# Performance work log

Measured on AMD Instinct MI355X. Metric: run time of the kernel, lower is better.

The kernel has to match this reference:

```python
import jax, jax.numpy as jnp
import numpy as np

N_NODES = 100000
N_EDGES = 1600000
N_GRAPHS = 1024
N_FEAT = 128
HID = 64
N_CLASSES = 16
N_CENT = 3  # centroids per class


def setup_inputs() -> dict:
    key = jax.random.key(0)
    ks = jax.random.split(key, 8)
    x = jax.random.normal(ks[0], (N_NODES, N_FEAT), dtype=jnp.float32)
    edge_index = jax.random.randint(ks[1], (2, N_EDGES), 0, N_NODES, dtype=jnp.int64)
    batch = jnp.sort(jax.random.randint(ks[2], (N_NODES,), 0, N_GRAPHS, dtype=jnp.int64))
    s = 1.0 / np.sqrt(N_FEAT)
    W1 = jax.random.normal(ks[3], (N_FEAT, HID), dtype=jnp.float32) * s
    W2 = jax.random.normal(ks[4], (HID, HID), dtype=jnp.float32) * (1.0 / np.sqrt(HID))
    W3 = jax.random.normal(ks[5], (HID, HID), dtype=jnp.float32) * (1.0 / np.sqrt(HID))
    b1 = jnp.zeros((HID,), jnp.float32)
    b2 = jnp.zeros((HID,), jnp.float32)
    b3 = jnp.zeros((HID,), jnp.float32)
    centroids = jax.random.normal(ks[6], (N_CLASSES * N_CENT, HID), dtype=jnp.float32)
    reject_bias = jnp.zeros((1,), jnp.float32)
    return {"x": x, "edge_index": edge_index, "batch": batch,
            "W1": W1, "b1": b1, "W2": W2, "b2": b2, "W3": W3, "b3": b3,
            "centroids": centroids, "reject_bias": reject_bias}


def _gcn_conv(x, W, b, src, dst, norm, n_nodes):
    # PyG GCNConv: out[dst] = sum_e norm_e * (x[src_e] @ W), + bias
    h = x @ W                      # [N, out]
    msg = h[src] * norm[:, None]   # [E+N, out] gather + scale
    out = jax.ops.segment_sum(msg, dst, num_segments=n_nodes)
    return out + b


def reference(x, edge_index, batch, W1, b1, W2, b2, W3, b3, centroids, reject_bias):
    n = x.shape[0]
    loops = jnp.arange(n, dtype=edge_index.dtype)
    src = jnp.concatenate([edge_index[0], loops])
    dst = jnp.concatenate([edge_index[1], loops])
    # symmetric normalization on A + I
    deg = jax.ops.segment_sum(jnp.ones_like(dst, dtype=x.dtype), dst, num_segments=n)
    dinv = jax.lax.rsqrt(jnp.maximum(deg, 1.0))
    norm = dinv[src] * dinv[dst]

    h = jax.nn.relu(_gcn_conv(x, W1, b1, src, dst, norm, n))  # dropout is identity at eval
    h = jax.nn.relu(_gcn_conv(h, W2, b2, src, dst, norm, n))
    h = _gcn_conv(h, W3, b3, src, dst, norm, n)

    # global mean pool over graphs in the batch
    summ = jax.ops.segment_sum(h, batch, num_segments=N_GRAPHS)          # [G, HID]
    cnt = jax.ops.segment_sum(jnp.ones((n,), h.dtype), batch, num_segments=N_GRAPHS)
    emb = summ / jnp.maximum(cnt, 1.0)[:, None]

    # centroid distance head: squared euclidean to all class centroids
    d = (jnp.sum(emb * emb, -1, keepdims=True)
         - 2.0 * emb @ centroids.T
         + jnp.sum(centroids * centroids, -1))                           # [G, 16*3]
    d_pc = jnp.min(d.reshape(-1, N_CLASSES, N_CENT), axis=-1)            # [G, 16]
    class_logits = -d_pc
    reject_logit = jnp.min(d_pc, axis=-1, keepdims=True) - reject_bias   # [G, 1]
    return jnp.concatenate([class_logits, reject_logit], axis=-1)        # [G, 17]
```

## Files before the change

### kernel.cpp

```cpp
#include <hip/hip_runtime.h>

#define HID 64
#define NCLS 16
#define NCENT 3
#define NCENTS (NCLS * NCENT)
#define BSHIFT 9
#define BINW (1 << BSHIFT)
#define NBINMAX 256
#define CHUNK 4096
#define EPT (CHUNK / 256)
#define NU 8

static inline int ceil_div(int a, int b) { return (a + b - 1) / b; }

__device__ inline unsigned short f2bf(float f) {
    unsigned int u = __float_as_uint(f);
    return (unsigned short)((u + 0x7FFFu + ((u >> 16) & 1u)) >> 16);
}
__device__ inline unsigned int pack2bf(float lo, float hi) {
    return (unsigned int)f2bf(lo) | ((unsigned int)f2bf(hi) << 16);
}
__device__ inline float bf2f(unsigned short h) {
    return __uint_as_float(((unsigned int)h) << 16);
}
__device__ inline float bflo(unsigned int u) { return __uint_as_float(u << 16); }
__device__ inline float bfhi(unsigned int u) { return __uint_as_float(u & 0xFFFF0000u); }

typedef short bf16x8 __attribute__((ext_vector_type(8)));
typedef float f32x4 __attribute__((ext_vector_type(4)));


__device__ void wprep_one(const float* __restrict__ W, unsigned short* __restrict__ Wh,
                          unsigned short* __restrict__ Wl, int K) {
    for (int idx = threadIdx.x; idx < K * 64; idx += 256) {
        int k = idx >> 6, colc = idx & 63;
        float f = W[idx];
        unsigned short h = f2bf(f);
        unsigned short lo = f2bf(f - bf2f(h));
        int kt = k >> 5, kin = k & 31, ct = colc >> 4;
        int ln = ((kin >> 3) << 4) | (colc & 15);
        int o = (((kt * 4 + ct) * 64) + ln) * 8 + (kin & 7);
        Wh[o] = h; Wl[o] = lo;
    }
}


__global__ void k_count_w(const int* __restrict__ dst, int* __restrict__ binCnt,
                          int E, int nbins,
                          const float* __restrict__ W1, const float* __restrict__ W2,
                          const float* __restrict__ W3,
                          unsigned short* __restrict__ W1h, unsigned short* __restrict__ W1l,
                          unsigned short* __restrict__ W2h, unsigned short* __restrict__ W2l,
                          unsigned short* __restrict__ W3h, unsigned short* __restrict__ W3l) {
    if (blockIdx.x >= gridDim.x - 3) {
        int w = blockIdx.x - (gridDim.x - 3);
        if (w == 0) wprep_one(W1, W1h, W1l, 128);
        else if (w == 1) wprep_one(W2, W2h, W2l, 64);
        else wprep_one(W3, W3h, W3l, 64);
        return;
    }
    __shared__ int c[NBINMAX];
    for (int i = threadIdx.x; i < nbins; i += 256) c[i] = 0;
    __syncthreads();
    int e = blockIdx.x * CHUNK + threadIdx.x;
#pragma unroll
    for (int j = 0; j < EPT; j++, e += 256)
        if (e < E) atomicAdd(&c[dst[e] >> BSHIFT], 1);
    __syncthreads();
    for (int i = threadIdx.x; i < nbins; i += 256)
        if (c[i] > 0) atomicAdd(&binCnt[i], c[i]);
}

__global__ void k_binoff(const int* __restrict__ binCnt, int* __restrict__ binBase,
                         int nbins, int E) {
    __shared__ int ts[NBINMAX];
    int t = threadIdx.x;
    int v = (t < nbins) ? binCnt[t] : 0;
    ts[t] = v;
    __syncthreads();
    for (int off = 1; off < NBINMAX; off <<= 1) {
        int x = (t >= off) ? ts[t - off] : 0;
        __syncthreads();
        ts[t] += x;
        __syncthreads();
    }
    if (t < nbins) binBase[t] = ts[t] - v;
    if (t == 0) binBase[nbins] = E;
}

__global__ __launch_bounds__(256) void k_bin(const int* __restrict__ src,
                                             const int* __restrict__ dst,
                                             const int* __restrict__ binBase,
                                             int* __restrict__ binCur,
                                             int2* __restrict__ binned,
                                             int E, int nbins) {
    __shared__ int cnt[NBINMAX], off[NBINMAX], gbase[NBINMAX];
    __shared__ int2 stage[CHUNK];
    const int c0 = blockIdx.x * CHUNK;
    const int tid = threadIdx.x;
    cnt[tid] = 0;
    __syncthreads();
    int sv[EPT], dv[EPT];
#pragma unroll
    for (int j = 0; j < EPT; j++) {
        int e = c0 + j * 256 + tid;
        dv[j] = -1;
        if (e < E) {
            sv[j] = src[e];
            dv[j] = dst[e];
            atomicAdd(&cnt[dv[j] >> BSHIFT], 1);
        }
    }
    __syncthreads();
    off[tid] = cnt[tid];
    __syncthreads();
    for (int o = 1; o < NBINMAX; o <<= 1) {
        int x = (tid >= o) ? off[tid - o] : 0;
        __syncthreads();
        off[tid] += x;
        __syncthreads();
    }
    int excl = off[tid] - cnt[tid];
    __syncthreads();
    off[tid] = excl;
    gbase[tid] = (tid < nbins && cnt[tid] > 0) ? atomicAdd(&binCur[tid], cnt[tid]) : 0;
    cnt[tid] = 0;
    __syncthreads();
#pragma unroll
    for (int j = 0; j < EPT; j++)
        if (dv[j] >= 0) {
            int b = dv[j] >> BSHIFT;
            int pos = off[b] + atomicAdd(&cnt[b], 1);
            stage[pos] = make_int2(sv[j], dv[j]);
        }
    __syncthreads();
    int tot = min(CHUNK, E - c0);
    for (int i = tid; i < tot; i += 256) {
        int2 v = stage[i];
        int b = v.y >> BSHIFT;
        binned[binBase[b] + gbase[b] + (i - off[b])] = v;
    }
}

__global__ __launch_bounds__(256) void k_fillc2(const int2* __restrict__ binned,
                                                const int* __restrict__ binBase,
                                                int* __restrict__ col,
                                                int* __restrict__ rs_out,
                                                int* __restrict__ deg_out,
                                                float* __restrict__ dinv_out, int N) {
    __shared__ int c[BINW];
    __shared__ int rsl[BINW];
    __shared__ int ts[256];
    int b = blockIdx.x;
    int s = binBase[b], e = binBase[b + 1];
    int n0 = b << BSHIFT;
    int t = threadIdx.x;
    c[2 * t] = 0; c[2 * t + 1] = 0;
    __syncthreads();
    for (int i = s + t; i < e; i += 256)
        atomicAdd(&c[binned[i].y - n0], 1);
    __syncthreads();
    int v0 = c[2 * t], v1 = c[2 * t + 1];
    ts[t] = v0 + v1;
    __syncthreads();
    for (int off = 1; off < 256; off <<= 1) {
        int x = (t >= off) ? ts[t - off] : 0;
        __syncthreads();
        ts[t] += x;
        __syncthreads();
    }
    int base = binBase[b] + ts[t] - (v0 + v1);
    rsl[2 * t] = base;
    rsl[2 * t + 1] = base + v0;
    int n = n0 + 2 * t;
    if (n < N) {
        deg_out[n] = v0; rs_out[n] = base;
        dinv_out[n] = rsqrtf((float)(v0 + 1));
    }
    if (n + 1 < N) {
        deg_out[n + 1] = v1; rs_out[n + 1] = base + v0;
        dinv_out[n + 1] = rsqrtf((float)(v1 + 1));
    }
    c[2 * t] = 0; c[2 * t + 1] = 0;
    __syncthreads();
    for (int i = s + t; i < e; i += 256) {
        int2 v = binned[i];
        int lo = v.y - n0;
        int pos = rsl[lo] + atomicAdd(&c[lo], 1);
        col[pos] = v.x;
    }
}


template <int K>
__global__ __launch_bounds__(256) void k_gemm_mfma(const float* __restrict__ Ain,
                                                   const unsigned short* __restrict__ Wh,
                                                   const unsigned short* __restrict__ Wl,
                                                   unsigned short* __restrict__ out,
                                                   const float* __restrict__ dinv, int N) {
    const int lane = threadIdx.x & 63;
    const int wave = threadIdx.x >> 6;
    const int row0 = blockIdx.x * 64 + wave * 16;
    int arow = row0 + (lane & 15);
    if (arow > N - 1) arow = N - 1;
    const int kb = (lane >> 4) * 8;

    f32x4 acc[4] = {};

#pragma unroll
    for (int kt = 0; kt < K / 32; ++kt) {
        bf16x8 ah, al;
        const float* ap = Ain + (size_t)arow * K + kt * 32 + kb;
        float4 f0 = *(const float4*)ap;
        float4 f1 = *(const float4*)(ap + 4);
        float fv[8] = {f0.x, f0.y, f0.z, f0.w, f1.x, f1.y, f1.z, f1.w};
#pragma unroll
        for (int j = 0; j < 8; ++j) {
            unsigned short h = f2bf(fv[j]);
            ah[j] = (short)h;
            al[j] = (short)f2bf(fv[j] - bf2f(h));
        }
#pragma unroll
        for (int ct = 0; ct < 4; ++ct) {
            const size_t wo = ((size_t)(kt * 4 + ct) * 64 + lane) * 8;
            bf16x8 wh = *(const bf16x8*)(Wh + wo);
            bf16x8 wl = *(const bf16x8*)(Wl + wo);
            acc[ct] = __builtin_amdgcn_mfma_f32_16x16x32_bf16(ah, wh, acc[ct], 0, 0, 0);
            acc[ct] = __builtin_amdgcn_mfma_f32_16x16x32_bf16(al, wh, acc[ct], 0, 0, 0);
            acc[ct] = __builtin_amdgcn_mfma_f32_16x16x32_bf16(ah, wl, acc[ct], 0, 0, 0);
        }
    }

    const int rb = row0 + (lane >> 4) * 4;
    const int cb = lane & 15;
#pragma unroll
    for (int i = 0; i < 4; ++i) {
        int row = rb + i;
        if (row < N) {
            float d = dinv[row];
#pragma unroll
            for (int ct = 0; ct < 4; ++ct)
                out[(size_t)row * HID + ct * 16 + cb] = f2bf(d * acc[ct][i]);
        }
    }
}


__global__ __launch_bounds__(256) void k_aggf(const unsigned short* __restrict__ tin,
                                              unsigned short* __restrict__ tout,
                                              const int* __restrict__ rs,
                                              const int* __restrict__ deg,
                                              const int* __restrict__ col,
                                              const float* __restrict__ dinv,
                                              const float* __restrict__ bias,
                                              const unsigned short* __restrict__ Wh,
                                              const unsigned short* __restrict__ Wl,
                                              int N) {
    __shared__ unsigned int tl[32][36];
    const int tid = threadIdx.x;
    const int lane = tid & 63;
    const int wave = tid >> 6;
    const int group = tid >> 3;
    const int l = tid & 7;
    int node = blockIdx.x * 32 + group;
    int cnode = node < N ? node : N - 1;

    float di = dinv[cnode];
    uint4 tb = ((const uint4*)(tin + (size_t)cnode * HID))[l];
    float a0 = bflo(tb.x), a1 = bfhi(tb.x);
    float a2 = bflo(tb.y), a3 = bfhi(tb.y);
    float a4 = bflo(tb.z), a5 = bfhi(tb.z);
    float a6 = bflo(tb.w), a7 = bfhi(tb.w);

    int beg = rs[cnode];
    int cnt = deg[cnode];
    int last = beg + cnt - 1;
    const int gbase = lane & 56;
    for (int e = 0; e < cnt; e += NU) {
        int idx = beg + e + l;
        int cv = col[idx < last ? idx : last];
        int sv[NU];
#pragma unroll
        for (int j = 0; j < NU; j++) sv[j] = __shfl(cv, gbase + j, 64);
        uint4 vv[NU];
#pragma unroll
        for (int j = 0; j < NU; j++) vv[j] = ((const uint4*)(tin + (size_t)sv[j] * HID))[l];
#pragma unroll
        for (int j = 0; j < NU; j++) {
            a0 += bflo(vv[j].x); a1 += bfhi(vv[j].x);
            a2 += bflo(vv[j].y); a3 += bfhi(vv[j].y);
            a4 += bflo(vv[j].z); a5 += bfhi(vv[j].z);
            a6 += bflo(vv[j].w); a7 += bfhi(vv[j].w);
        }
    }
    int pad = (NU - (cnt & (NU - 1))) & (NU - 1);
    if (cnt > 0 && pad > 0) {
        float fp = (float)pad;
        uint4 vl = ((const uint4*)(tin + (size_t)col[last] * HID))[l];
        a0 = fmaf(-fp, bflo(vl.x), a0); a1 = fmaf(-fp, bfhi(vl.x), a1);
        a2 = fmaf(-fp, bflo(vl.y), a2); a3 = fmaf(-fp, bfhi(vl.y), a3);
        a4 = fmaf(-fp, bflo(vl.z), a4); a5 = fmaf(-fp, bfhi(vl.z), a5);
        a6 = fmaf(-fp, bflo(vl.w), a6); a7 = fmaf(-fp, bfhi(vl.w), a7);
    }
    float4 b0 = ((const float4*)bias)[2 * l];
    float4 b1 = ((const float4*)bias)[2 * l + 1];
    a0 = fmaxf(fmaf(di, a0, b0.x), 0.f); a1 = fmaxf(fmaf(di, a1, b0.y), 0.f);
    a2 = fmaxf(fmaf(di, a2, b0.z), 0.f); a3 = fmaxf(fmaf(di, a3, b0.w), 0.f);
    a4 = fmaxf(fmaf(di, a4, b1.x), 0.f); a5 = fmaxf(fmaf(di, a5, b1.y), 0.f);
    a6 = fmaxf(fmaf(di, a6, b1.z), 0.f); a7 = fmaxf(fmaf(di, a7, b1.w), 0.f);

    uint4 o;
    o.x = pack2bf(a0, a1); o.y = pack2bf(a2, a3);
    o.z = pack2bf(a4, a5); o.w = pack2bf(a6, a7);
    *(uint4*)&tl[group][4 * l] = o;
    __syncthreads();

    const int row0 = (wave >> 1) * 16;
    const int ctb = (wave & 1) * 2;
    const int arow = row0 + (lane & 15);
    const int am = lane >> 4;

    f32x4 acc[2] = {};
#pragma unroll
    for (int kt = 0; kt < 2; ++kt) {
        bf16x8 ah = *(const bf16x8*)&tl[arow][kt * 16 + 4 * am];
#pragma unroll
        for (int c = 0; c < 2; ++c) {
            const size_t wo = ((size_t)(kt * 4 + ctb + c) * 64 + lane) * 8;
            bf16x8 wh = *(const bf16x8*)(Wh + wo);
            bf16x8 wl = *(const bf16x8*)(Wl + wo);
            acc[c] = __builtin_amdgcn_mfma_f32_16x16x32_bf16(ah, wh, acc[c], 0, 0, 0);
            acc[c] = __builtin_amdgcn_mfma_f32_16x16x32_bf16(ah, wl, acc[c], 0, 0, 0);
        }
    }

    const int rb = row0 + (lane >> 4) * 4;
    const int cb = lane & 15;
#pragma unroll
    for (int i = 0; i < 4; ++i) {
        int gnode = blockIdx.x * 32 + rb + i;
        if (gnode < N) {
            float d2 = dinv[gnode];
#pragma unroll
            for (int c = 0; c < 2; ++c)
                tout[(size_t)gnode * HID + (ctb + c) * 16 + cb] = f2bf(d2 * acc[c][i]);
        }
    }
}


__global__ void k_agg(const unsigned short* __restrict__ tin,
                      unsigned short* __restrict__ out,
                      const int* __restrict__ rs, const int* __restrict__ deg,
                      const int* __restrict__ col,
                      const float* __restrict__ dinv, const float* __restrict__ bias,
                      int N) {
    int node = (blockIdx.x * blockDim.x + threadIdx.x) >> 3;
    int l = threadIdx.x & 7;
    if (node >= N) return;
    int lane = threadIdx.x & 63;
    float di = dinv[node];
    uint4 tb = ((const uint4*)(tin + (size_t)node * HID))[l];
    float a0 = bflo(tb.x), a1 = bfhi(tb.x);
    float a2 = bflo(tb.y), a3 = bfhi(tb.y);
    float a4 = bflo(tb.z), a5 = bfhi(tb.z);
    float a6 = bflo(tb.w), a7 = bfhi(tb.w);

    int beg = rs[node];
    int cnt = deg[node];
    int last = beg + cnt - 1;
    const int gbase = lane & 56;
    for (int e = 0; e < cnt; e += NU) {
        int idx = beg + e + l;
        int cv = col[idx < last ? idx : last];
        int sv[NU];
#pragma unroll
        for (int j = 0; j < NU; j++) sv[j] = __shfl(cv, gbase + j, 64);
        uint4 vv[NU];
#pragma unroll
        for (int j = 0; j < NU; j++) vv[j] = ((const uint4*)(tin + (size_t)sv[j] * HID))[l];
#pragma unroll
        for (int j = 0; j < NU; j++) {
            a0 += bflo(vv[j].x); a1 += bfhi(vv[j].x);
            a2 += bflo(vv[j].y); a3 += bfhi(vv[j].y);
            a4 += bflo(vv[j].z); a5 += bfhi(vv[j].z);
            a6 += bflo(vv[j].w); a7 += bfhi(vv[j].w);
        }
    }
    int pad = (NU - (cnt & (NU - 1))) & (NU - 1);
    if (cnt > 0 && pad > 0) {
        float fp = (float)pad;
        uint4 vl = ((const uint4*)(tin + (size_t)col[last] * HID))[l];
        a0 = fmaf(-fp, bflo(vl.x), a0); a1 = fmaf(-fp, bfhi(vl.x), a1);
        a2 = fmaf(-fp, bflo(vl.y), a2); a3 = fmaf(-fp, bfhi(vl.y), a3);
        a4 = fmaf(-fp, bflo(vl.z), a4); a5 = fmaf(-fp, bfhi(vl.z), a5);
        a6 = fmaf(-fp, bflo(vl.w), a6); a7 = fmaf(-fp, bfhi(vl.w), a7);
    }
    float4 b0 = ((const float4*)bias)[2 * l];
    float4 b1 = ((const float4*)bias)[2 * l + 1];
    a0 = fmaf(di, a0, b0.x); a1 = fmaf(di, a1, b0.y);
    a2 = fmaf(di, a2, b0.z); a3 = fmaf(di, a3, b0.w);
    a4 = fmaf(di, a4, b1.x); a5 = fmaf(di, a5, b1.y);
    a6 = fmaf(di, a6, b1.z); a7 = fmaf(di, a7, b1.w);
    uint4 o;
    o.x = pack2bf(a0, a1); o.y = pack2bf(a2, a3);
    o.z = pack2bf(a4, a5); o.w = pack2bf(a6, a7);
    ((uint4*)(out + (size_t)node * HID))[l] = o;
}


__global__ void k_pool_head(const unsigned short* __restrict__ h,
                            const int* __restrict__ batch,
                            const float* __restrict__ cent, const float* __restrict__ rbias,
                            float* __restrict__ out, int N) {
    int g = blockIdx.x;
    int lo = 0, hi = N;
    while (lo < hi) { int mid = (lo + hi) >> 1; if (batch[mid] < g) lo = mid + 1; else hi = mid; }
    int s = lo;
    lo = 0; hi = N;
    while (lo < hi) { int mid = (lo + hi) >> 1; if (batch[mid] < g + 1) lo = mid + 1; else hi = mid; }
    int e = lo;

    __shared__ float part[4][HID];
    __shared__ float embS[HID];
    __shared__ float dS[NCENTS];
    __shared__ float dpcS[NCLS];

    int lane = threadIdx.x & 63, wid = threadIdx.x >> 6;
    float acc = 0.0f;
    for (int i = s + wid; i < e; i += 4) acc += bf2f(h[(size_t)i * HID + lane]);
    part[wid][lane] = acc;
    __syncthreads();
    if (wid == 0) {
        float v = part[0][lane] + part[1][lane] + part[2][lane] + part[3][lane];
        embS[lane] = v / fmaxf((float)(e - s), 1.0f);
    }
    __syncthreads();
    if (threadIdx.x < NCENTS) {
        const float* c = cent + threadIdx.x * HID;
        float d = 0.0f;
        for (int k = 0; k < HID; k++) { float df = embS[k] - c[k]; d = fmaf(df, df, d); }
        dS[threadIdx.x] = d;
    }
    __syncthreads();
    if (threadIdx.x < NCLS) {
        float m = fminf(dS[threadIdx.x * 3],
                        fminf(dS[threadIdx.x * 3 + 1], dS[threadIdx.x * 3 + 2]));
        dpcS[threadIdx.x] = m;
        out[g * (NCLS + 1) + threadIdx.x] = -m;
    }
    __syncthreads();
    if (threadIdx.x == 0) {
        float m = dpcS[0];
        for (int i = 1; i < NCLS; i++) m = fminf(m, dpcS[i]);
        out[g * (NCLS + 1) + NCLS] = m - rbias[0];
    }
}


extern "C" void kernel_launch(void* const* d_in, const int* in_sizes, int n_in,
                              void* d_out, int out_size, void* d_ws, size_t ws_size,
                              hipStream_t stream) {
    const float* x    = (const float*)d_in[0];
    const int*   ei   = (const int*)d_in[1];
    const int*   bat  = (const int*)d_in[2];
    const float* W1   = (const float*)d_in[3];
    const float* b1   = (const float*)d_in[4];
    const float* W2   = (const float*)d_in[5];
    const float* b2   = (const float*)d_in[6];
    const float* W3   = (const float*)d_in[7];
    const float* b3   = (const float*)d_in[8];
    const float* cent = (const float*)d_in[9];
    const float* rb   = (const float*)d_in[10];
    float* out = (float*)d_out;

    const int N = in_sizes[0] / 128;
    const int E = in_sizes[1] / 2;
    const int nbins = (N + BINW - 1) >> BSHIFT;

    char* p = (char*)d_ws;
    unsigned short* T0 = (unsigned short*)p; p += (size_t)N * HID * 2;
    unsigned short* T1 = (unsigned short*)p; p += (size_t)N * HID * 2;
    int2*  binned = (int2*)p;  p += (size_t)E * 8;
    int*   col    = (int*)p;   p += (size_t)E * 4;
    float* dinv   = (float*)p; p += (size_t)N * 4;
    int*   rs     = (int*)p;   p += (size_t)N * 4;
    int*   deg    = (int*)p;   p += (size_t)N * 4;
    int*   binBase= (int*)p;   p += (NBINMAX + 2) * 4;
    int*   binCnt = (int*)p;   p += NBINMAX * 4;
    int*   binCur = (int*)p;   p += NBINMAX * 4;
    p = (char*)(((uintptr_t)p + 15) & ~(uintptr_t)15);
    unsigned short* W1h = (unsigned short*)p; p += 8192 * 2;
    unsigned short* W1l = (unsigned short*)p; p += 8192 * 2;
    unsigned short* W2h = (unsigned short*)p; p += 4096 * 2;
    unsigned short* W2l = (unsigned short*)p; p += 4096 * 2;
    unsigned short* W3h = (unsigned short*)p; p += 4096 * 2;
    unsigned short* W3l = (unsigned short*)p; p += 4096 * 2;

    hipMemsetAsync(binCnt, 0, 2 * NBINMAX * 4, stream);

    const int nEB = ceil_div(E, CHUNK);
    k_count_w<<<nEB + 3, 256, 0, stream>>>(ei + E, binCnt, E, nbins,
                                           W1, W2, W3, W1h, W1l, W2h, W2l, W3h, W3l);
    k_binoff<<<1, 256, 0, stream>>>(binCnt, binBase, nbins, E);
    k_bin<<<nEB, 256, 0, stream>>>(ei, ei + E, binBase, binCur, binned, E, nbins);
    k_fillc2<<<nbins, 256, 0, stream>>>(binned, binBase, col, rs, deg, dinv, N);

    k_gemm_mfma<128><<<ceil_div(N, 64), 256, 0, stream>>>(x, W1h, W1l, T0, dinv, N);
    k_aggf<<<ceil_div(N, 32), 256, 0, stream>>>(T0, T1, rs, deg, col, dinv, b1, W2h, W2l, N);
    k_aggf<<<ceil_div(N, 32), 256, 0, stream>>>(T1, T0, rs, deg, col, dinv, b2, W3h, W3l, N);
    k_agg<<<ceil_div(N * 8, 256), 256, 0, stream>>>(T0, T1, rs, deg, col, dinv, b3, N);

    k_pool_head<<<1024, 256, 0, stream>>>(T1, bat, cent, rb, out, N);
}
```

Baseline: 307.4 us.

## Sort nodes by degree for load-balanced aggregation and prefetch next column indices

Builds a degree histogram during CSR fill, scans it, and scatters nodes into a degree-sorted permutation. The aggregation kernels then process nodes in that order, so the 8 node groups in a wavefront have similar edge counts and less loop divergence. The aggregation loop also prefetches the next chunk of column indices before the feature gathers. In exchange it adds two small kernels plus an extra indirection, and destroys the spatial locality of writes and self-feature reads.

```diff
diff --git a/kernel.cpp b/kernel.cpp
--- a/kernel.cpp
+++ b/kernel.cpp
@@ -10,6 +10,7 @@
 #define CHUNK 4096
 #define EPT (CHUNK / 256)
 #define NU 8
+#define NDB 64
 
 static inline int ceil_div(int a, int b) { return (a + b - 1) / b; }
 
@@ -147,15 +148,18 @@
                                                 int* __restrict__ col,
                                                 int* __restrict__ rs_out,
                                                 int* __restrict__ deg_out,
-                                                float* __restrict__ dinv_out, int N) {
+                                                float* __restrict__ dinv_out,
+                                                int* __restrict__ degHist, int N) {
     __shared__ int c[BINW];
     __shared__ int rsl[BINW];
     __shared__ int ts[256];
+    __shared__ int dh[NDB];
     int b = blockIdx.x;
     int s = binBase[b], e = binBase[b + 1];
     int n0 = b << BSHIFT;
     int t = threadIdx.x;
     c[2 * t] = 0; c[2 * t + 1] = 0;
+    if (t < NDB) dh[t] = 0;
     __syncthreads();
     for (int i = s + t; i < e; i += 256)
         atomicAdd(&c[binned[i].y - n0], 1);
@@ -176,10 +180,12 @@
     if (n < N) {
         deg_out[n] = v0; rs_out[n] = base;
         dinv_out[n] = rsqrtf((float)(v0 + 1));
+        atomicAdd(&dh[v0 < NDB - 1 ? v0 : NDB - 1], 1);
     }
     if (n + 1 < N) {
         deg_out[n + 1] = v1; rs_out[n + 1] = base + v0;
         dinv_out[n + 1] = rsqrtf((float)(v1 + 1));
+        atomicAdd(&dh[v1 < NDB - 1 ? v1 : NDB - 1], 1);
     }
     c[2 * t] = 0; c[2 * t + 1] = 0;
     __syncthreads();
@@ -188,6 +194,50 @@
         int lo = v.y - n0;
         int pos = rsl[lo] + atomicAdd(&c[lo], 1);
         col[pos] = v.x;
+    }
+    __syncthreads();
+    if (t < NDB && dh[t] > 0) atomicAdd(&degHist[t], dh[t]);
+}
+
+
+__global__ void k_dscan(const int* __restrict__ degHist, int* __restrict__ bucketCur) {
+    __shared__ int ts[NDB];
+    int t = threadIdx.x;
+    int v = degHist[t];
+    ts[t] = v;
+    __syncthreads();
+    for (int o = 1; o < NDB; o <<= 1) {
+        int x = (t >= o) ? ts[t - o] : 0;
+        __syncthreads();
+        ts[t] += x;
+        __syncthreads();
+    }
+    bucketCur[t] = ts[t] - v;
+}
+
+
+__global__ __launch_bounds__(256) void k_pscatter(const int* __restrict__ deg,
+                                                  int* __restrict__ bucketCur,
+                                                  int* __restrict__ perm, int N) {
+    __shared__ int cnt[NDB], gb[NDB];
+    int t = threadIdx.x;
+    int node = blockIdx.x * 256 + t;
+    if (t < NDB) cnt[t] = 0;
+    __syncthreads();
+    int d = -1;
+    if (node < N) {
+        d = deg[node]; d = d < NDB - 1 ? d : NDB - 1;
+        atomicAdd(&cnt[d], 1);
+    }
+    __syncthreads();
+    if (t < NDB) {
+        gb[t] = cnt[t] > 0 ? atomicAdd(&bucketCur[t], cnt[t]) : 0;
+        cnt[t] = 0;
+    }
+    __syncthreads();
+    if (node < N) {
+        int pos = gb[d] + atomicAdd(&cnt[d], 1);
+        perm[pos] = node;
     }
 }
 
@@ -255,6 +305,7 @@
                                               const float* __restrict__ bias,
                                               const unsigned short* __restrict__ Wh,
                                               const unsigned short* __restrict__ Wl,
+                                              const int* __restrict__ perm,
                                               int N) {
     __shared__ unsigned int tl[32][36];
     const int tid = threadIdx.x;
@@ -262,8 +313,8 @@
     const int wave = tid >> 6;
     const int group = tid >> 3;
     const int l = tid & 7;
-    int node = blockIdx.x * 32 + group;
-    int cnode = node < N ? node : N - 1;
+    int gi = blockIdx.x * 32 + group;
+    int cnode = perm[gi < N ? gi : N - 1];
 
     float di = dinv[cnode];
     uint4 tb = ((const uint4*)(tin + (size_t)cnode * HID))[l];
@@ -276,15 +327,18 @@
     int cnt = deg[cnode];
     int last = beg + cnt - 1;
     const int gbase = lane & 56;
+    int pidx = beg + l;
+    int cv = (cnt > 0) ? col[pidx < last ? pidx : last] : 0;
     for (int e = 0; e < cnt; e += NU) {
-        int idx = beg + e + l;
-        int cv = col[idx < last ? idx : last];
         int sv[NU];
 #pragma unroll
         for (int j = 0; j < NU; j++) sv[j] = __shfl(cv, gbase + j, 64);
+        int nidx = beg + e + NU + l;
+        int cvn = col[nidx < last ? nidx : last];
         uint4 vv[NU];
 #pragma unroll
         for (int j = 0; j < NU; j++) vv[j] = ((const uint4*)(tin + (size_t)sv[j] * HID))[l];
+        cv = cvn;
 #pragma unroll
         for (int j = 0; j < NU; j++) {
             a0 += bflo(vv[j].x); a1 += bfhi(vv[j].x);
@@ -338,8 +392,9 @@
     const int cb = lane & 15;
 #pragma unroll
     for (int i = 0; i < 4; ++i) {
-        int gnode = blockIdx.x * 32 + rb + i;
-        if (gnode < N) {
+        int oidx = blockIdx.x * 32 + rb + i;
+        if (oidx < N) {
+            int gnode = perm[oidx];
             float d2 = dinv[gnode];
 #pragma unroll
             for (int c = 0; c < 2; ++c)
@@ -354,10 +409,11 @@
                       const int* __restrict__ rs, const int* __restrict__ deg,
                       const int* __restrict__ col,
                       const float* __restrict__ dinv, const float* __restrict__ bias,
-                      int N) {
-    int node = (blockIdx.x * blockDim.x + threadIdx.x) >> 3;
+                      const int* __restrict__ perm, int N) {
+    int gi = (blockIdx.x * blockDim.x + threadIdx.x) >> 3;
     int l = threadIdx.x & 7;
-    if (node >= N) return;
+    if (gi >= N) return;
+    int node = perm[gi];
     int lane = threadIdx.x & 63;
     float di = dinv[node];
     uint4 tb = ((const uint4*)(tin + (size_t)node * HID))[l];
@@ -370,15 +426,18 @@
     int cnt = deg[node];
     int last = beg + cnt - 1;
     const int gbase = lane & 56;
+    int pidx = beg + l;
+    int cv = (cnt > 0) ? col[pidx < last ? pidx : last] : 0;
     for (int e = 0; e < cnt; e += NU) {
-        int idx = beg + e + l;
-        int cv = col[idx < last ? idx : last];
         int sv[NU];
 #pragma unroll
         for (int j = 0; j < NU; j++) sv[j] = __shfl(cv, gbase + j, 64);
+        int nidx = beg + e + NU + l;
+        int cvn = col[nidx < last ? nidx : last];
         uint4 vv[NU];
 #pragma unroll
         for (int j = 0; j < NU; j++) vv[j] = ((const uint4*)(tin + (size_t)sv[j] * HID))[l];
+        cv = cvn;
 #pragma unroll
         for (int j = 0; j < NU; j++) {
             a0 += bflo(vv[j].x); a1 += bfhi(vv[j].x);
@@ -486,9 +545,12 @@
     float* dinv   = (float*)p; p += (size_t)N * 4;
     int*   rs     = (int*)p;   p += (size_t)N * 4;
     int*   deg    = (int*)p;   p += (size_t)N * 4;
+    int*   perm   = (int*)p;   p += (size_t)N * 4;
     int*   binBase= (int*)p;   p += (NBINMAX + 2) * 4;
     int*   binCnt = (int*)p;   p += NBINMAX * 4;
     int*   binCur = (int*)p;   p += NBINMAX * 4;
+    int*   degHist= (int*)p;   p += NDB * 4;
+    int*   bucketCur = (int*)p; p += NDB * 4;
     p = (char*)(((uintptr_t)p + 15) & ~(uintptr_t)15);
     unsigned short* W1h = (unsigned short*)p; p += 8192 * 2;
     unsigned short* W1l = (unsigned short*)p; p += 8192 * 2;
@@ -497,19 +559,21 @@
     unsigned short* W3h = (unsigned short*)p; p += 4096 * 2;
     unsigned short* W3l = (unsigned short*)p; p += 4096 * 2;
 
-    hipMemsetAsync(binCnt, 0, 2 * NBINMAX * 4, stream);
+    hipMemsetAsync(binCnt, 0, (2 * NBINMAX + NDB) * 4, stream);
 
     const int nEB = ceil_div(E, CHUNK);
     k_count_w<<<nEB + 3, 256, 0, stream>>>(ei + E, binCnt, E, nbins,
                                            W1, W2, W3, W1h, W1l, W2h, W2l, W3h, W3l);
     k_binoff<<<1, 256, 0, stream>>>(binCnt, binBase, nbins, E);
     k_bin<<<nEB, 256, 0, stream>>>(ei, ei + E, binBase, binCur, binned, E, nbins);
-    k_fillc2<<<nbins, 256, 0, stream>>>(binned, binBase, col, rs, deg, dinv, N);
+    k_fillc2<<<nbins, 256, 0, stream>>>(binned, binBase, col, rs, deg, dinv, degHist, N);
+    k_dscan<<<1, NDB, 0, stream>>>(degHist, bucketCur);
+    k_pscatter<<<ceil_div(N, 256), 256, 0, stream>>>(deg, bucketCur, perm, N);
 
     k_gemm_mfma<128><<<ceil_div(N, 64), 256, 0, stream>>>(x, W1h, W1l, T0, dinv, N);
-    k_aggf<<<ceil_div(N, 32), 256, 0, stream>>>(T0, T1, rs, deg, col, dinv, b1, W2h, W2l, N);
-    k_aggf<<<ceil_div(N, 32), 256, 0, stream>>>(T1, T0, rs, deg, col, dinv, b2, W3h, W3l, N);
-    k_agg<<<ceil_div(N * 8, 256), 256, 0, stream>>>(T0, T1, rs, deg, col, dinv, b3, N);
+    k_aggf<<<ceil_div(N, 32), 256, 0, stream>>>(T0, T1, rs, deg, col, dinv, b1, W2h, W2l, perm, N);
+    k_aggf<<<ceil_div(N, 32), 256, 0, stream>>>(T1, T0, rs, deg, col, dinv, b2, W3h, W3l, perm, N);
+    k_agg<<<ceil_div(N * 8, 256), 256, 0, stream>>>(T0, T1, rs, deg, col, dinv, b3, perm, N);
 
     k_pool_head<<<1024, 256, 0, stream>>>(T1, bat, cent, rb, out, N);
 }
```

Result: slower. 328.0 us (+6.7%).

## Fuse final aggregation with mean pooling via atomics and prefetch column indices

Applied to the files above, without the earlier changes.

The last GCN aggregation now accumulates each node's result straight into per-graph float sums and counts with atomicAdd, instead of writing a bf16 node tensor that a separate pool kernel re-reads after two binary searches per graph. This removes one full N×64 write and read plus the pooling pass, and a small head kernel finishes the centroid distances. Both aggregation loops also prefetch the next batch of column indices before issuing the feature gathers, to hide index-load latency. In exchange it adds heavy atomic traffic on 1024×64 sums, 8 atomics per thread, makes the summation order nondeterministic, and hardcodes the graph count.

```diff
diff --git a/kernel.cpp b/kernel.cpp
--- a/kernel.cpp
+++ b/kernel.cpp
@@ -4,6 +4,7 @@
 #define NCLS 16
 #define NCENT 3
 #define NCENTS (NCLS * NCENT)
+#define NGR 1024
 #define BSHIFT 9
 #define BINW (1 << BSHIFT)
 #define NBINMAX 256
@@ -276,15 +277,18 @@
     int cnt = deg[cnode];
     int last = beg + cnt - 1;
     const int gbase = lane & 56;
+    int pidx = beg + l;
+    int cv = (cnt > 0) ? col[pidx < last ? pidx : last] : 0;
     for (int e = 0; e < cnt; e += NU) {
-        int idx = beg + e + l;
-        int cv = col[idx < last ? idx : last];
         int sv[NU];
 #pragma unroll
         for (int j = 0; j < NU; j++) sv[j] = __shfl(cv, gbase + j, 64);
+        int nidx = beg + e + NU + l;
+        int cvn = col[nidx < last ? nidx : last];
         uint4 vv[NU];
 #pragma unroll
         for (int j = 0; j < NU; j++) vv[j] = ((const uint4*)(tin + (size_t)sv[j] * HID))[l];
+        cv = cvn;
 #pragma unroll
         for (int j = 0; j < NU; j++) {
             a0 += bflo(vv[j].x); a1 += bfhi(vv[j].x);
@@ -349,12 +353,13 @@
 }
 
 
-__global__ void k_agg(const unsigned short* __restrict__ tin,
-                      unsigned short* __restrict__ out,
-                      const int* __restrict__ rs, const int* __restrict__ deg,
-                      const int* __restrict__ col,
-                      const float* __restrict__ dinv, const float* __restrict__ bias,
-                      int N) {
+__global__ void k_agg_pool(const unsigned short* __restrict__ tin,
+                           const int* __restrict__ rs, const int* __restrict__ deg,
+                           const int* __restrict__ col,
+                           const float* __restrict__ dinv, const float* __restrict__ bias,
+                           const int* __restrict__ batch,
+                           float* __restrict__ embSum, int* __restrict__ embCnt,
+                           int N) {
     int node = (blockIdx.x * blockDim.x + threadIdx.x) >> 3;
     int l = threadIdx.x & 7;
     if (node >= N) return;
@@ -370,15 +375,18 @@
     int cnt = deg[node];
     int last = beg + cnt - 1;
     const int gbase = lane & 56;
+    int pidx = beg + l;
+    int cv = (cnt > 0) ? col[pidx < last ? pidx : last] : 0;
     for (int e = 0; e < cnt; e += NU) {
-        int idx = beg + e + l;
-        int cv = col[idx < last ? idx : last];
         int sv[NU];
 #pragma unroll
         for (int j = 0; j < NU; j++) sv[j] = __shfl(cv, gbase + j, 64);
+        int nidx = beg + e + NU + l;
+        int cvn = col[nidx < last ? nidx : last];
         uint4 vv[NU];
 #pragma unroll
         for (int j = 0; j < NU; j++) vv[j] = ((const uint4*)(tin + (size_t)sv[j] * HID))[l];
+        cv = cvn;
 #pragma unroll
         for (int j = 0; j < NU; j++) {
             a0 += bflo(vv[j].x); a1 += bfhi(vv[j].x);
@@ -402,55 +410,42 @@
     a2 = fmaf(di, a2, b0.z); a3 = fmaf(di, a3, b0.w);
     a4 = fmaf(di, a4, b1.x); a5 = fmaf(di, a5, b1.y);
     a6 = fmaf(di, a6, b1.z); a7 = fmaf(di, a7, b1.w);
-    uint4 o;
-    o.x = pack2bf(a0, a1); o.y = pack2bf(a2, a3);
-    o.z = pack2bf(a4, a5); o.w = pack2bf(a6, a7);
-    ((uint4*)(out + (size_t)node * HID))[l] = o;
-}
-
-
-__global__ void k_pool_head(const unsigned short* __restrict__ h,
-                            const int* __restrict__ batch,
-                            const float* __restrict__ cent, const float* __restrict__ rbias,
-                            float* __restrict__ out, int N) {
+
+    int g = batch[node];
+    float* es = embSum + (size_t)g * HID + 8 * l;
+    atomicAdd(es + 0, a0); atomicAdd(es + 1, a1);
+    atomicAdd(es + 2, a2); atomicAdd(es + 3, a3);
+    atomicAdd(es + 4, a4); atomicAdd(es + 5, a5);
+    atomicAdd(es + 6, a6); atomicAdd(es + 7, a7);
+    if (l == 0) atomicAdd(&embCnt[g], 1);
+}
+
+
+__global__ void k_head(const float* __restrict__ embSum, const int* __restrict__ embCnt,
+                       const float* __restrict__ cent, const float* __restrict__ rbias,
+                       float* __restrict__ out) {
     int g = blockIdx.x;
-    int lo = 0, hi = N;
-    while (lo < hi) { int mid = (lo + hi) >> 1; if (batch[mid] < g) lo = mid + 1; else hi = mid; }
-    int s = lo;
-    lo = 0; hi = N;
-    while (lo < hi) { int mid = (lo + hi) >> 1; if (batch[mid] < g + 1) lo = mid + 1; else hi = mid; }
-    int e = lo;
-
-    __shared__ float part[4][HID];
-    __shared__ float embS[HID];
+    int t = threadIdx.x;
+    __shared__ float emb[HID];
     __shared__ float dS[NCENTS];
     __shared__ float dpcS[NCLS];
-
-    int lane = threadIdx.x & 63, wid = threadIdx.x >> 6;
-    float acc = 0.0f;
-    for (int i = s + wid; i < e; i += 4) acc += bf2f(h[(size_t)i * HID + lane]);
-    part[wid][lane] = acc;
-    __syncthreads();
-    if (wid == 0) {
-        float v = part[0][lane] + part[1][lane] + part[2][lane] + part[3][lane];
-        embS[lane] = v / fmaxf((float)(e - s), 1.0f);
-    }
-    __syncthreads();
-    if (threadIdx.x < NCENTS) {
-        const float* c = cent + threadIdx.x * HID;
+    float cntf = fmaxf((float)embCnt[g], 1.0f);
+    emb[t] = embSum[(size_t)g * HID + t] / cntf;
+    __syncthreads();
+    if (t < NCENTS) {
+        const float* c = cent + t * HID;
         float d = 0.0f;
-        for (int k = 0; k < HID; k++) { float df = embS[k] - c[k]; d = fmaf(df, df, d); }
-        dS[threadIdx.x] = d;
-    }
-    __syncthreads();
-    if (threadIdx.x < NCLS) {
-        float m = fminf(dS[threadIdx.x * 3],
-                        fminf(dS[threadIdx.x * 3 + 1], dS[threadIdx.x * 3 + 2]));
-        dpcS[threadIdx.x] = m;
-        out[g * (NCLS + 1) + threadIdx.x] = -m;
-    }
-    __syncthreads();
-    if (threadIdx.x == 0) {
+        for (int k = 0; k < HID; k++) { float df = emb[k] - c[k]; d = fmaf(df, df, d); }
+        dS[t] = d;
+    }
+    __syncthreads();
+    if (t < NCLS) {
+        float m = fminf(dS[t * 3], fminf(dS[t * 3 + 1], dS[t * 3 + 2]));
+        dpcS[t] = m;
+        out[g * (NCLS + 1) + t] = -m;
+    }
+    __syncthreads();
+    if (t == 0) {
         float m = dpcS[0];
         for (int i = 1; i < NCLS; i++) m = fminf(m, dpcS[i]);
         out[g * (NCLS + 1) + NCLS] = m - rbias[0];
@@ -489,6 +484,8 @@
     int*   binBase= (int*)p;   p += (NBINMAX + 2) * 4;
     int*   binCnt = (int*)p;   p += NBINMAX * 4;
     int*   binCur = (int*)p;   p += NBINMAX * 4;
+    float* embSum = (float*)p; p += (size_t)NGR * HID * 4;
+    int*   embCnt = (int*)p;   p += NGR * 4;
     p = (char*)(((uintptr_t)p + 15) & ~(uintptr_t)15);
     unsigned short* W1h = (unsigned short*)p; p += 8192 * 2;
     unsigned short* W1l = (unsigned short*)p; p += 8192 * 2;
@@ -497,7 +494,7 @@
     unsigned short* W3h = (unsigned short*)p; p += 4096 * 2;
     unsigned short* W3l = (unsigned short*)p; p += 4096 * 2;
 
-    hipMemsetAsync(binCnt, 0, 2 * NBINMAX * 4, stream);
+    hipMemsetAsync(binCnt, 0, (2 * NBINMAX + NGR * HID + NGR) * 4, stream);
 
     const int nEB = ceil_div(E, CHUNK);
     k_count_w<<<nEB + 3, 256, 0, stream>>>(ei + E, binCnt, E, nbins,
@@ -509,7 +506,8 @@
     k_gemm_mfma<128><<<ceil_div(N, 64), 256, 0, stream>>>(x, W1h, W1l, T0, dinv, N);
     k_aggf<<<ceil_div(N, 32), 256, 0, stream>>>(T0, T1, rs, deg, col, dinv, b1, W2h, W2l, N);
     k_aggf<<<ceil_div(N, 32), 256, 0, stream>>>(T1, T0, rs, deg, col, dinv, b2, W3h, W3l, N);
-    k_agg<<<ceil_div(N * 8, 256), 256, 0, stream>>>(T0, T1, rs, deg, col, dinv, b3, N);
-
-    k_pool_head<<<1024, 256, 0, stream>>>(T1, bat, cent, rb, out, N);
-}
+    k_agg_pool<<<ceil_div(N * 8, 256), 256, 0, stream>>>(T0, rs, deg, col, dinv, b3,
+                                                         bat, embSum, embCnt, N);
+
+    k_head<<<NGR, 64, 0, stream>>>(embSum, embCnt, cent, rb, out);
+}
```

New measurement: 573.4 us. 86.6% more time.

## Prefetch next neighbor indices in aggregation and split final agg by feature quarters

Applied to the files above, without the earlier changes.

In the fused aggregation kernel, the column indices for the next batch of neighbours are now loaded before the current gathers, so the dependent index load overlaps the feature loads. The final aggregation kernel is restructured: each node uses 2 threads instead of 8, and the 64 features are split into four 16-feature slices handled by separate block groups. This puts more nodes in each wave and shrinks the gather footprint per block, which may improve cache locality. In exchange, the index lists are re-read four times, per-node degree imbalance inside a wave grows, and an extra index prefetch runs past the end of the loop.

```diff
diff --git a/kernel.cpp b/kernel.cpp
--- a/kernel.cpp
+++ b/kernel.cpp
@@ -276,15 +276,18 @@
     int cnt = deg[cnode];
     int last = beg + cnt - 1;
     const int gbase = lane & 56;
+    int pidx = beg + l;
+    int cv = (cnt > 0) ? col[pidx < last ? pidx : last] : 0;
     for (int e = 0; e < cnt; e += NU) {
-        int idx = beg + e + l;
-        int cv = col[idx < last ? idx : last];
         int sv[NU];
 #pragma unroll
         for (int j = 0; j < NU; j++) sv[j] = __shfl(cv, gbase + j, 64);
+        int nidx = beg + e + NU + l;
+        int cvn = col[nidx < last ? nidx : last];
         uint4 vv[NU];
 #pragma unroll
         for (int j = 0; j < NU; j++) vv[j] = ((const uint4*)(tin + (size_t)sv[j] * HID))[l];
+        cv = cvn;
 #pragma unroll
         for (int j = 0; j < NU; j++) {
             a0 += bflo(vv[j].x); a1 += bfhi(vv[j].x);
@@ -349,18 +352,26 @@
 }
 
 
-__global__ void k_agg(const unsigned short* __restrict__ tin,
-                      unsigned short* __restrict__ out,
-                      const int* __restrict__ rs, const int* __restrict__ deg,
-                      const int* __restrict__ col,
-                      const float* __restrict__ dinv, const float* __restrict__ bias,
-                      int N) {
-    int node = (blockIdx.x * blockDim.x + threadIdx.x) >> 3;
-    int l = threadIdx.x & 7;
-    if (node >= N) return;
-    int lane = threadIdx.x & 63;
+__global__ __launch_bounds__(256) void k_agg4(const unsigned short* __restrict__ tin,
+                                              unsigned short* __restrict__ out,
+                                              const int* __restrict__ rs,
+                                              const int* __restrict__ deg,
+                                              const int* __restrict__ col,
+                                              const float* __restrict__ dinv,
+                                              const float* __restrict__ bias,
+                                              int N, int nodeBlocks) {
+    const int q = blockIdx.x / nodeBlocks;
+    const int nb = blockIdx.x - q * nodeBlocks;
+    const int tid = threadIdx.x;
+    const int lane = tid & 63;
+    const int l = tid & 1;
+    int node = nb * 128 + (tid >> 1);
+    bool active = node < N;
+    if (!active) node = N - 1;
+    const int fb = q * 16 + l * 8;
+
     float di = dinv[node];
-    uint4 tb = ((const uint4*)(tin + (size_t)node * HID))[l];
+    uint4 tb = *(const uint4*)(tin + (size_t)node * HID + fb);
     float a0 = bflo(tb.x), a1 = bfhi(tb.x);
     float a2 = bflo(tb.y), a3 = bfhi(tb.y);
     float a4 = bflo(tb.z), a5 = bfhi(tb.z);
@@ -369,16 +380,29 @@
     int beg = rs[node];
     int cnt = deg[node];
     int last = beg + cnt - 1;
-    const int gbase = lane & 56;
+    const int gl = lane & 62;
+    int sown[4];
+#pragma unroll
+    for (int k = 0; k < 4; k++) {
+        int idx = beg + 4 * l + k;
+        sown[k] = (cnt > 0) ? col[idx < last ? idx : last] : 0;
+    }
     for (int e = 0; e < cnt; e += NU) {
-        int idx = beg + e + l;
-        int cv = col[idx < last ? idx : last];
         int sv[NU];
 #pragma unroll
-        for (int j = 0; j < NU; j++) sv[j] = __shfl(cv, gbase + j, 64);
+        for (int j = 0; j < NU; j++) sv[j] = __shfl(sown[j & 3], gl + (j >> 2), 64);
+        int nown[4];
+#pragma unroll
+        for (int k = 0; k < 4; k++) {
+            int idx = beg + e + NU + 4 * l + k;
+            nown[k] = col[idx < last ? idx : last];
+        }
         uint4 vv[NU];
 #pragma unroll
-        for (int j = 0; j < NU; j++) vv[j] = ((const uint4*)(tin + (size_t)sv[j] * HID))[l];
+        for (int j = 0; j < NU; j++)
+            vv[j] = *(const uint4*)(tin + (size_t)sv[j] * HID + fb);
+#pragma unroll
+        for (int k = 0; k < 4; k++) sown[k] = nown[k];
 #pragma unroll
         for (int j = 0; j < NU; j++) {
             a0 += bflo(vv[j].x); a1 += bfhi(vv[j].x);
@@ -390,22 +414,24 @@
     int pad = (NU - (cnt & (NU - 1))) & (NU - 1);
     if (cnt > 0 && pad > 0) {
         float fp = (float)pad;
-        uint4 vl = ((const uint4*)(tin + (size_t)col[last] * HID))[l];
+        uint4 vl = *(const uint4*)(tin + (size_t)col[last] * HID + fb);
         a0 = fmaf(-fp, bflo(vl.x), a0); a1 = fmaf(-fp, bfhi(vl.x), a1);
         a2 = fmaf(-fp, bflo(vl.y), a2); a3 = fmaf(-fp, bfhi(vl.y), a3);
         a4 = fmaf(-fp, bflo(vl.z), a4); a5 = fmaf(-fp, bfhi(vl.z), a5);
         a6 = fmaf(-fp, bflo(vl.w), a6); a7 = fmaf(-fp, bfhi(vl.w), a7);
     }
-    float4 b0 = ((const float4*)bias)[2 * l];
-    float4 b1 = ((const float4*)bias)[2 * l + 1];
+    float4 b0 = ((const float4*)(bias + fb))[0];
+    float4 b1 = ((const float4*)(bias + fb))[1];
     a0 = fmaf(di, a0, b0.x); a1 = fmaf(di, a1, b0.y);
     a2 = fmaf(di, a2, b0.z); a3 = fmaf(di, a3, b0.w);
     a4 = fmaf(di, a4, b1.x); a5 = fmaf(di, a5, b1.y);
     a6 = fmaf(di, a6, b1.z); a7 = fmaf(di, a7, b1.w);
-    uint4 o;
-    o.x = pack2bf(a0, a1); o.y = pack2bf(a2, a3);
-    o.z = pack2bf(a4, a5); o.w = pack2bf(a6, a7);
-    ((uint4*)(out + (size_t)node * HID))[l] = o;
+    if (active) {
+        uint4 o;
+        o.x = pack2bf(a0, a1); o.y = pack2bf(a2, a3);
+        o.z = pack2bf(a4, a5); o.w = pack2bf(a6, a7);
+        *(uint4*)(out + (size_t)node * HID + fb) = o;
+    }
 }
 
 
@@ -509,7 +535,8 @@
     k_gemm_mfma<128><<<ceil_div(N, 64), 256, 0, stream>>>(x, W1h, W1l, T0, dinv, N);
     k_aggf<<<ceil_div(N, 32), 256, 0, stream>>>(T0, T1, rs, deg, col, dinv, b1, W2h, W2l, N);
     k_aggf<<<ceil_div(N, 32), 256, 0, stream>>>(T1, T0, rs, deg, col, dinv, b2, W3h, W3l, N);
-    k_agg<<<ceil_div(N * 8, 256), 256, 0, stream>>>(T0, T1, rs, deg, col, dinv, b3, N);
+    const int nodeBlocks = ceil_div(N, 128);
+    k_agg4<<<4 * nodeBlocks, 256, 0, stream>>>(T0, T1, rs, deg, col, dinv, b3, N, nodeBlocks);
 
     k_pool_head<<<1024, 256, 0, stream>>>(T1, bat, cent, rb, out, N);
 }
```

Measured after the change: 384.2 us. 25.0% more time.
